# Kernel optimization log

Measured on AMD Instinct MI355X. Metric: run time of the kernel, lower is better.

## Reference

```python
import jax, jax.numpy as jnp
import numpy as np

LOG_2PI = np.float32(np.log(2.0 * np.pi))
NEG_BIG = np.float32(-9e15)


def setup_inputs() -> dict:
    key = jax.random.key(0)
    ks = jax.random.split(key, 8)
    N, F_in, F_out, H = 8192, 512, 128, 16
    x = jax.random.normal(ks[0], (N, F_in), dtype=jnp.float32)
    adj = jax.random.randint(ks[1], (N, N), 0, 2, dtype=jnp.int32)
    # xavier_uniform-ish init for W (gain 1.414)
    lim = np.float32(1.414 * np.sqrt(6.0 / (F_in + F_out)))
    W = jax.random.uniform(ks[2], (F_in, F_out), jnp.float32, -lim, lim)
    # VariationalAttentionNet params: lin1(2*F_out -> H), lin21/lin22(H -> 1)
    w1 = jax.random.normal(ks[3], (H, 2 * F_out), dtype=jnp.float32) * 0.05
    b1 = jnp.zeros((H,), jnp.float32)
    w21 = jax.random.normal(ks[4], (1, H), dtype=jnp.float32) * 0.05
    b21 = jnp.zeros((1,), jnp.float32)
    w22 = jax.random.normal(ks[5], (1, H), dtype=jnp.float32) * 0.05
    b22 = jnp.zeros((1,), jnp.float32)
    return {"x": x, "adj": adj, "W": W, "w1": w1, "b1": b1,
            "w21": w21, "b21": b21, "w22": w22, "b22": b22}


def reference(x, adj, W, w1, b1, w21, b21, w22, b22):
    # h = x @ W  [N, F_out]
    h = x @ W
    # VariationalAttentionNet(h, h), eval mode: z = mu
    u = jax.nn.relu(jnp.concatenate([h, h], axis=1) @ w1.T + b1)  # [N, H]
    mu = u @ w21.T + b21   # [N, 1]
    lv = u @ w22.T + b22   # [N, 1]
    sigma = jax.nn.softplus(lv)
    z = mu
    # qmp = -(log p(z) - log q(z)); with z = mu, log q(mu) = -log(sigma) - 0.5*log(2pi)
    log_p = jnp.sum(-0.5 * z * z - 0.5 * LOG_2PI)
    log_q = jnp.sum(-jnp.log(sigma) - 0.5 * LOG_2PI)
    qmp = log_q - log_p
    # per-node score z broadcast across row, masked by adjacency, row softmax
    scores = jnp.where(adj > 0, z, NEG_BIG)          # [N, N]
    attention = jax.nn.softmax(scores, axis=1)       # [N, N] (dropout off in eval)
    h_prime = attention @ h                          # [N, F_out]
    return jax.nn.elu(h_prime), qmp
```

## Files before the change

kernel.cpp:

```cpp
#include <hip/hip_runtime.h>

typedef unsigned int u32;
typedef unsigned short u16;

#define NN 8192
#define FIN 512
#define FOUT 128
#define NH 16
#define BK 64
#define BKA 256

typedef float f32x16 __attribute__((ext_vector_type(16)));
typedef __bf16 bf16x8 __attribute__((ext_vector_type(8)));

union PackAB { u32 u[4]; bf16x8 v; };

__device__ __forceinline__ u32 rne_hi(u32 u) {
  return u + (0x7FFFu + ((u >> 16) & 1u));
}
__device__ __forceinline__ u16 f32_to_bf16(float f) {
  return (u16)(rne_hi(__float_as_uint(f)) >> 16);
}

__global__ __launch_bounds__(256) void prep_kernel(
    const float* __restrict__ W, const float* __restrict__ w1,
    u16* __restrict__ WT, float* __restrict__ w1s) {
  int b = blockIdx.x, t = threadIdx.x;
  if (b < 256) {
    int o = b * 256 + t;
    int n = o >> 9, k = o & 511;
    WT[o] = f32_to_bf16(W[k * FOUT + n]);
  } else {
    for (int e = t; e < NH * FOUT; e += 256) {
      int k = e >> 7, f = e & 127;
      w1s[e] = w1[k * 256 + f] + w1[k * 256 + 128 + f];
    }
  }
}

__global__ __launch_bounds__(256) void h_fused_kernel(
    const float* __restrict__ x, const u16* __restrict__ WT,
    const float* __restrict__ b1, const float* __restrict__ w21,
    const float* __restrict__ b21, const float* __restrict__ w22,
    const float* __restrict__ b22, const float* __restrict__ w1s,
    u16* __restrict__ HTf, float* __restrict__ qpart) {
  __shared__ union {
    struct { u16 aS[32 * BK]; u16 bS[128 * BK]; } g;
    float hs[32][FOUT + 4];
  } S;
  __shared__ float w1l[NH][FOUT + 4];
  __shared__ float us[32][NH + 1];
  int t = threadIdx.x;
  int w = t >> 6, l = t & 63;
  int m = l & 31, kh = l >> 5;
  int i0 = blockIdx.x * 32;

  int arow = t >> 4, acol = (t & 15) * 4;
  int ac = (t & 15) >> 1, ah = t & 1;
  int aoff0 = arow * BK + ((ac ^ (arow & 7)) << 3) + ah * 4;
  int aoff1 = (arow + 16) * BK + ((ac ^ ((arow + 16) & 7)) << 3) + ah * 4;
  const float* ap0 = x + (size_t)(i0 + arow) * FIN + acol;
  const float* ap1 = ap0 + (size_t)16 * FIN;
  int hr = t >> 3, hc = t & 7;
  const u16* bp0 = WT + (size_t)hr * FIN + hc * 8;
  int boff[4];
#pragma unroll
  for (int p = 0; p < 4; ++p) {
    int r = hr + 32 * p;
    boff[p] = r * BK + ((hc ^ (r & 7)) << 3);
  }
  int aro = m * BK, am7 = m & 7;
  int nB = w * 32 + m;
  int bro = nB * BK, bm7 = nB & 7;

  float4 xa[8], xb[8];
#pragma unroll
  for (int o = 0; o < 8; ++o) {
    xa[o] = *(const float4*)(ap0 + o * BK);
    xb[o] = *(const float4*)(ap1 + o * BK);
  }
  uint4 hC[4], hN[4];
#pragma unroll
  for (int j = 0; j < 4; ++j) hC[j] = *(const uint4*)(bp0 + (size_t)(32 * j) * FIN);
  bp0 += BK;

  f32x16 acc;
#pragma unroll
  for (int r = 0; r < 16; ++r) acc[r] = 0.0f;

#pragma unroll
  for (int o = 0; o < 8; ++o) {
    if (o) __syncthreads();
    uint2 w0, w1v;
    w0.x = (rne_hi(__float_as_uint(xa[o].y)) & 0xFFFF0000u) | (rne_hi(__float_as_uint(xa[o].x)) >> 16);
    w0.y = (rne_hi(__float_as_uint(xa[o].w)) & 0xFFFF0000u) | (rne_hi(__float_as_uint(xa[o].z)) >> 16);
    w1v.x = (rne_hi(__float_as_uint(xb[o].y)) & 0xFFFF0000u) | (rne_hi(__float_as_uint(xb[o].x)) >> 16);
    w1v.y = (rne_hi(__float_as_uint(xb[o].w)) & 0xFFFF0000u) | (rne_hi(__float_as_uint(xb[o].z)) >> 16);
    *(uint2*)&S.g.aS[aoff0] = w0;
    *(uint2*)&S.g.aS[aoff1] = w1v;
#pragma unroll
    for (int j = 0; j < 4; ++j) *(uint4*)&S.g.bS[boff[j]] = hC[j];
    __syncthreads();
    if (o + 1 < 8) {
#pragma unroll
      for (int j = 0; j < 4; ++j) hN[j] = *(const uint4*)(bp0 + (size_t)(32 * j) * FIN);
      bp0 += BK;
    }
#pragma unroll
    for (int s = 0; s < BK; s += 16) {
      int cA = (s >> 3) + kh;
      PackAB pa, pb;
      pa.v = *(const bf16x8*)&S.g.aS[aro + ((cA ^ am7) << 3)];
      pb.v = *(const bf16x8*)&S.g.bS[bro + ((cA ^ bm7) << 3)];
      acc = __builtin_amdgcn_mfma_f32_32x32x16_bf16(pa.v, pb.v, acc, 0, 0, 0);
    }
    if (o + 1 < 8) {
#pragma unroll
      for (int j = 0; j < 4; ++j) hC[j] = hN[j];
    }
  }
  __syncthreads();
  {
    int col = w * 32 + m;
#pragma unroll
    for (int r = 0; r < 16; ++r) {
      int row = (r & 3) + 8 * (r >> 2) + 4 * kh;
      S.hs[row][col] = acc[r];
    }
  }
  for (int e = t; e < NH * FOUT; e += 256) w1l[e >> 7][e & 127] = w1s[e];
  __syncthreads();
  {
    int n = t & 127, g2 = t >> 7;
#pragma unroll
    for (int gg = 0; gg < 2; ++gg) {
      int g = g2 + 2 * gg;
      int k16 = (i0 >> 4) + (g >> 1), khh = g & 1;
      u32 p[4];
#pragma unroll
      for (int j = 0; j < 4; ++j) {
        u16 lo = f32_to_bf16(S.hs[g * 8 + 2 * j][n]);
        u16 hi = f32_to_bf16(S.hs[g * 8 + 2 * j + 1][n]);
        p[j] = (u32)lo | ((u32)hi << 16);
      }
      uint4 st; st.x = p[0]; st.y = p[1]; st.z = p[2]; st.w = p[3];
      size_t off = ((size_t)(k16 * 4 + (n >> 5)) * 64 + khh * 32 + (n & 31)) * 8;
      *(uint4*)(HTf + off) = st;
    }
  }
  {
    int i = t >> 3, p = t & 7;
    float s0 = b1[p], s1 = b1[p + 8];
#pragma unroll 4
    for (int f = 0; f < FOUT; ++f) {
      float hv = S.hs[i][f];
      s0 = fmaf(hv, w1l[p][f], s0);
      s1 = fmaf(hv, w1l[p + 8][f], s1);
    }
    us[i][p] = fmaxf(s0, 0.0f);
    us[i][p + 8] = fmaxf(s1, 0.0f);
  }
  __syncthreads();
  if (t < 32) {
    float mu = b21[0], lv = b22[0];
#pragma unroll
    for (int k = 0; k < NH; ++k) {
      mu = fmaf(us[t][k], w21[k], mu);
      lv = fmaf(us[t][k], w22[k], lv);
    }
    float sp = fmaxf(lv, 0.0f) + log1pf(expf(-fabsf(lv)));
    float q = 0.5f * mu * mu - logf(sp);
#pragma unroll
    for (int off = 16; off; off >>= 1) q += __shfl_down(q, off);
    if (t == 0) qpart[blockIdx.x] = q;
  }
}

__global__ __launch_bounds__(256) void attn_kernel(
    const int* __restrict__ adj, const u16* __restrict__ HTf,
    const float* __restrict__ qpart, float* __restrict__ out) {
  __shared__ u16 aS[32 * BKA];
  __shared__ float dinv[32];
  int t = threadIdx.x;
  int w = t >> 6, l = t & 63;
  int m = l & 31, kh = l >> 5;
  int i0 = blockIdx.x * 32;

  int ar = t >> 3, lc = t & 7;
  const int* apb = adj + (size_t)(i0 + ar) * NN + lc * 4;
  int woff[8];
#pragma unroll
  for (int q = 0; q < 8; ++q) {
    int c = q * 4 + (lc >> 1);
    woff[q] = ar * 256 + (((c ^ ar) & 31) << 3) + (lc & 1) * 4;
  }
  const u16* bp = HTf + (size_t)(w * 64 + l) * 8;

  f32x16 acc;
#pragma unroll
  for (int r = 0; r < 16; ++r) acc[r] = 0.0f;
  u32 degacc = 0;

  const int nslab = NN / BKA;
  int4 aC[8], aN[8];
#pragma unroll
  for (int q = 0; q < 8; ++q) aC[q] = *(const int4*)(apb + q * 32);
  apb += BKA;

  for (int o = 0; o < nslab; ++o) {
    if (o) __syncthreads();
#pragma unroll
    for (int q = 0; q < 8; ++q) {
      u32 p0 = ((u32)aC[q].y << 16) | (u32)aC[q].x;
      u32 p1 = ((u32)aC[q].w << 16) | (u32)aC[q].z;
      degacc += p0 + p1;
      uint2 wv; wv.x = p0 * 0x3F80u; wv.y = p1 * 0x3F80u;
      *(uint2*)&aS[woff[q]] = wv;
    }
    __syncthreads();
    if (o + 1 < nslab) {
#pragma unroll
      for (int q = 0; q < 8; ++q) aN[q] = *(const int4*)(apb + q * 32);
      apb += BKA;
    }
    {
      bf16x8 bF[4];
#pragma unroll
      for (int j = 0; j < 4; ++j) bF[j] = *(const bf16x8*)(bp + j * 2048);
#pragma unroll
      for (int k16 = 0; k16 < 16; k16 += 4) {
        bf16x8 bN[4];
        if (k16 + 4 < 16) {
#pragma unroll
          for (int j = 0; j < 4; ++j)
            bN[j] = *(const bf16x8*)(bp + (k16 + 4 + j) * 2048);
        }
#pragma unroll
        for (int j = 0; j < 4; ++j) {
          int cc = (k16 + j) * 2 + kh;
          PackAB pa;
          pa.v = *(const bf16x8*)&aS[m * 256 + (((cc ^ m) & 31) << 3)];
          acc = __builtin_amdgcn_mfma_f32_32x32x16_bf16(pa.v, bF[j], acc, 0, 0, 0);
        }
#pragma unroll
        for (int j = 0; j < 4; ++j) bF[j] = bN[j];
      }
    }
    bp += (size_t)16 * 2048;
#pragma unroll
    for (int q = 0; q < 8; ++q) aC[q] = aN[q];
  }
  u32 d = (degacc & 0xFFFFu) + (degacc >> 16);
  d += __shfl_down(d, 4);
  d += __shfl_down(d, 2);
  d += __shfl_down(d, 1);
  if (lc == 0) dinv[ar] = d ? 1.0f / (float)d : 0.0f;
  __syncthreads();
  int col = w * 32 + m;
#pragma unroll
  for (int r = 0; r < 16; ++r) {
    int row = (r & 3) + 8 * (r >> 2) + 4 * kh;
    float v = acc[r] * dinv[row];
    v = v > 0.0f ? v : expm1f(v);
    out[(size_t)(i0 + row) * FOUT + col] = v;
  }
  if (blockIdx.x == 0 && t < 64) {
    float v = qpart[t] + qpart[t + 64] + qpart[t + 128] + qpart[t + 192];
#pragma unroll
    for (int off = 32; off; off >>= 1) v += __shfl_down(v, off);
    if (t == 0) out[(size_t)NN * FOUT] = v;
  }
}

extern "C" void kernel_launch(void* const* d_in, const int* in_sizes, int n_in,
                              void* d_out, int out_size, void* d_ws, size_t ws_size,
                              hipStream_t stream) {
  (void)in_sizes; (void)n_in; (void)out_size; (void)ws_size;
  const float* x   = (const float*)d_in[0];
  const int*   adj = (const int*)d_in[1];
  const float* W   = (const float*)d_in[2];
  const float* w1  = (const float*)d_in[3];
  const float* b1  = (const float*)d_in[4];
  const float* w21 = (const float*)d_in[5];
  const float* b21 = (const float*)d_in[6];
  const float* w22 = (const float*)d_in[7];
  const float* b22 = (const float*)d_in[8];
  float* out = (float*)d_out;

  char* ws = (char*)d_ws;
  u16*   HTf  = (u16*)ws;   ws += (size_t)NN * FOUT * 2;
  u16*   WT   = (u16*)ws;   ws += (size_t)FOUT * FIN * 2;
  float* w1s  = (float*)ws; ws += NH * FOUT * 4;
  float* qpart= (float*)ws;

  prep_kernel<<<257, 256, 0, stream>>>(W, w1, WT, w1s);
  h_fused_kernel<<<256, 256, 0, stream>>>(x, WT, b1, w21, b21, w22, b22, w1s, HTf, qpart);
  attn_kernel<<<256, 256, 0, stream>>>(adj, HTf, qpart, out);
}
```

Measured before the change: 505.9 us.

## Split attention K dimension across four wave groups per block with LDS reduction

Each attention block now runs 1024 threads as four 256-thread groups. Each group handles a quarter of the neighbor dimension with its own LDS slab, and the partial accumulators and degree counts are combined through shared memory before normalization and ELU. The aim is more waves per CU, so more adj loads are in flight on this memory-bound 256MB adjacency stream with only 256 blocks. The cost is 64KB of LDS per block, an extra reduction pass with two barriers, and launch bounds that may limit registers.

```diff
diff --git a/kernel.cpp b/kernel.cpp
--- a/kernel.cpp
+++ b/kernel.cpp
@@ -176,32 +176,35 @@
   }
 }
 
-__global__ __launch_bounds__(256) void attn_kernel(
+__global__ __launch_bounds__(1024, 4) void attn_kernel(
     const int* __restrict__ adj, const u16* __restrict__ HTf,
     const float* __restrict__ qpart, float* __restrict__ out) {
-  __shared__ u16 aS[32 * BKA];
-  __shared__ float dinv[32];
+  __shared__ u16 aS[4 * 32 * BKA];
+  __shared__ float degp[4][32];
   int t = threadIdx.x;
-  int w = t >> 6, l = t & 63;
+  int g = t >> 8, tl = t & 255;
+  int w = tl >> 6, l = tl & 63;
   int m = l & 31, kh = l >> 5;
   int i0 = blockIdx.x * 32;
-
-  int ar = t >> 3, lc = t & 7;
-  const int* apb = adj + (size_t)(i0 + ar) * NN + lc * 4;
+  int k0 = g * (NN / 4);
+
+  int ar = tl >> 3, lc = tl & 7;
+  const int* apb = adj + (size_t)(i0 + ar) * NN + k0 + lc * 4;
+  int goff = g * 32 * BKA;
   int woff[8];
 #pragma unroll
   for (int q = 0; q < 8; ++q) {
     int c = q * 4 + (lc >> 1);
-    woff[q] = ar * 256 + (((c ^ ar) & 31) << 3) + (lc & 1) * 4;
-  }
-  const u16* bp = HTf + (size_t)(w * 64 + l) * 8;
+    woff[q] = goff + ar * 256 + (((c ^ ar) & 31) << 3) + (lc & 1) * 4;
+  }
+  const u16* bp = HTf + ((size_t)(k0 >> 4) * 4 * 64 + (size_t)(w * 64 + l)) * 8;
 
   f32x16 acc;
 #pragma unroll
   for (int r = 0; r < 16; ++r) acc[r] = 0.0f;
   u32 degacc = 0;
 
-  const int nslab = NN / BKA;
+  const int nslab = (NN / 4) / BKA;
   int4 aC[8], aN[8];
 #pragma unroll
   for (int q = 0; q < 8; ++q) aC[q] = *(const int4*)(apb + q * 32);
@@ -239,7 +242,7 @@
         for (int j = 0; j < 4; ++j) {
           int cc = (k16 + j) * 2 + kh;
           PackAB pa;
-          pa.v = *(const bf16x8*)&aS[m * 256 + (((cc ^ m) & 31) << 3)];
+          pa.v = *(const bf16x8*)&aS[goff + m * 256 + (((cc ^ m) & 31) << 3)];
           acc = __builtin_amdgcn_mfma_f32_32x32x16_bf16(pa.v, bF[j], acc, 0, 0, 0);
         }
 #pragma unroll
@@ -254,15 +257,38 @@
   d += __shfl_down(d, 4);
   d += __shfl_down(d, 2);
   d += __shfl_down(d, 1);
-  if (lc == 0) dinv[ar] = d ? 1.0f / (float)d : 0.0f;
-  __syncthreads();
-  int col = w * 32 + m;
-#pragma unroll
-  for (int r = 0; r < 16; ++r) {
-    int row = (r & 3) + 8 * (r >> 2) + 4 * kh;
-    float v = acc[r] * dinv[row];
-    v = v > 0.0f ? v : expm1f(v);
-    out[(size_t)(i0 + row) * FOUT + col] = v;
+  if (lc == 0) degp[g][ar] = (float)d;
+  __syncthreads();
+  {
+    float* accS = (float*)&aS[goff];
+    int col = w * 32 + m;
+#pragma unroll
+    for (int r = 0; r < 16; ++r) {
+      int row = (r & 3) + 8 * (r >> 2) + 4 * kh;
+      accS[row * 128 + col] = acc[r];
+    }
+  }
+  __syncthreads();
+  {
+    int idx = t * 4;
+    int row = idx >> 7;
+    const float* r0 = (const float*)aS;
+    float4 v0 = *(const float4*)(r0 + idx);
+    float4 v1 = *(const float4*)(r0 + 4096 + idx);
+    float4 v2 = *(const float4*)(r0 + 8192 + idx);
+    float4 v3 = *(const float4*)(r0 + 12288 + idx);
+    float deg = degp[0][row] + degp[1][row] + degp[2][row] + degp[3][row];
+    float rd = deg != 0.0f ? 1.0f / deg : 0.0f;
+    float4 o;
+    o.x = (v0.x + v1.x + v2.x + v3.x) * rd;
+    o.y = (v0.y + v1.y + v2.y + v3.y) * rd;
+    o.z = (v0.z + v1.z + v2.z + v3.z) * rd;
+    o.w = (v0.w + v1.w + v2.w + v3.w) * rd;
+    o.x = o.x > 0.0f ? o.x : expm1f(o.x);
+    o.y = o.y > 0.0f ? o.y : expm1f(o.y);
+    o.z = o.z > 0.0f ? o.z : expm1f(o.z);
+    o.w = o.w > 0.0f ? o.w : expm1f(o.w);
+    *(float4*)(out + (size_t)(i0 + row) * FOUT + (idx & 127)) = o;
   }
   if (blockIdx.x == 0 && t < 64) {
     float v = qpart[t] + qpart[t + 64] + qpart[t + 128] + qpart[t + 192];
@@ -295,5 +321,5 @@
 
   prep_kernel<<<257, 256, 0, stream>>>(W, w1, WT, w1s);
   h_fused_kernel<<<256, 256, 0, stream>>>(x, WT, b1, w21, b21, w22, b22, w1s, HTf, qpart);
-  attn_kernel<<<256, 256, 0, stream>>>(adj, HTf, qpart, out);
-}
+  attn_kernel<<<256, 1024, 0, stream>>>(adj, HTf, qpart, out);
+}
```

Result: faster. 449.9 us (-11.1%).

## Split attention K dimension across waves with direct register A fragments

Applied to the files above, without the earlier changes.

The attention kernel now uses 512 threads, and each of its 8 waves handles a separate K-range of the adjacency row block while computing all 128 output columns. Each wave builds its MFMA A operands straight from global adjacency loads into registers, which removes the LDS staging and the per-slab barriers. Partial accumulators and degrees are combined with shared-memory atomics before a vectorized ELU epilogue. The cost is more accumulator registers, uncoalesced per-row adjacency loads, and atomic reduction traffic in LDS.

```diff
diff --git a/kernel.cpp b/kernel.cpp
--- a/kernel.cpp
+++ b/kernel.cpp
@@ -8,7 +8,6 @@
 #define FOUT 128
 #define NH 16
 #define BK 64
-#define BKA 256
 
 typedef float f32x16 __attribute__((ext_vector_type(16)));
 typedef __bf16 bf16x8 __attribute__((ext_vector_type(8)));
@@ -176,93 +175,112 @@
   }
 }
 
-__global__ __launch_bounds__(256) void attn_kernel(
+__global__ __launch_bounds__(512, 2) void attn_kernel(
     const int* __restrict__ adj, const u16* __restrict__ HTf,
     const float* __restrict__ qpart, float* __restrict__ out) {
-  __shared__ u16 aS[32 * BKA];
-  __shared__ float dinv[32];
+  __shared__ float accS[32 * FOUT];
+  __shared__ u32 degS[32];
   int t = threadIdx.x;
   int w = t >> 6, l = t & 63;
   int m = l & 31, kh = l >> 5;
   int i0 = blockIdx.x * 32;
 
-  int ar = t >> 3, lc = t & 7;
-  const int* apb = adj + (size_t)(i0 + ar) * NN + lc * 4;
-  int woff[8];
-#pragma unroll
-  for (int q = 0; q < 8; ++q) {
-    int c = q * 4 + (lc >> 1);
-    woff[q] = ar * 256 + (((c ^ ar) & 31) << 3) + (lc & 1) * 4;
-  }
-  const u16* bp = HTf + (size_t)(w * 64 + l) * 8;
-
-  f32x16 acc;
-#pragma unroll
-  for (int r = 0; r < 16; ++r) acc[r] = 0.0f;
+  for (int e = t; e < 32 * FOUT; e += 512) accS[e] = 0.0f;
+  if (t < 32) degS[t] = 0u;
+  __syncthreads();
+
+  int k0 = w * (NN / 8);
+  const int* ap = adj + (size_t)(i0 + m) * NN + k0 + kh * 8;
+  const u16* bp = HTf + (size_t)(k0 >> 4) * 2048 + (size_t)l * 8;
+
+  f32x16 acc[4];
+#pragma unroll
+  for (int nb = 0; nb < 4; ++nb)
+#pragma unroll
+    for (int r = 0; r < 16; ++r) acc[nb][r] = 0.0f;
   u32 degacc = 0;
 
-  const int nslab = NN / BKA;
-  int4 aC[8], aN[8];
-#pragma unroll
-  for (int q = 0; q < 8; ++q) aC[q] = *(const int4*)(apb + q * 32);
-  apb += BKA;
-
-  for (int o = 0; o < nslab; ++o) {
-    if (o) __syncthreads();
-#pragma unroll
-    for (int q = 0; q < 8; ++q) {
-      u32 p0 = ((u32)aC[q].y << 16) | (u32)aC[q].x;
-      u32 p1 = ((u32)aC[q].w << 16) | (u32)aC[q].z;
-      degacc += p0 + p1;
-      uint2 wv; wv.x = p0 * 0x3F80u; wv.y = p1 * 0x3F80u;
-      *(uint2*)&aS[woff[q]] = wv;
-    }
-    __syncthreads();
-    if (o + 1 < nslab) {
-#pragma unroll
-      for (int q = 0; q < 8; ++q) aN[q] = *(const int4*)(apb + q * 32);
-      apb += BKA;
+  int4 c0 = *(const int4*)(ap);
+  int4 c1 = *(const int4*)(ap + 4);
+  int4 c2 = *(const int4*)(ap + 16);
+  int4 c3 = *(const int4*)(ap + 20);
+  ap += 32;
+
+  for (int it = 0; it < 32; ++it) {
+    int4 n0, n1, n2, n3;
+    if (it + 1 < 32) {
+      n0 = *(const int4*)(ap);
+      n1 = *(const int4*)(ap + 4);
+      n2 = *(const int4*)(ap + 16);
+      n3 = *(const int4*)(ap + 20);
+      ap += 32;
     }
     {
-      bf16x8 bF[4];
-#pragma unroll
-      for (int j = 0; j < 4; ++j) bF[j] = *(const bf16x8*)(bp + j * 2048);
-#pragma unroll
-      for (int k16 = 0; k16 < 16; k16 += 4) {
-        bf16x8 bN[4];
-        if (k16 + 4 < 16) {
-#pragma unroll
-          for (int j = 0; j < 4; ++j)
-            bN[j] = *(const bf16x8*)(bp + (k16 + 4 + j) * 2048);
-        }
-#pragma unroll
-        for (int j = 0; j < 4; ++j) {
-          int cc = (k16 + j) * 2 + kh;
-          PackAB pa;
-          pa.v = *(const bf16x8*)&aS[m * 256 + (((cc ^ m) & 31) << 3)];
-          acc = __builtin_amdgcn_mfma_f32_32x32x16_bf16(pa.v, bF[j], acc, 0, 0, 0);
-        }
-#pragma unroll
-        for (int j = 0; j < 4; ++j) bF[j] = bN[j];
+      PackAB fa;
+      u32 p0 = ((u32)c0.y << 16) | (u32)c0.x;
+      u32 p1 = ((u32)c0.w << 16) | (u32)c0.z;
+      u32 p2 = ((u32)c1.y << 16) | (u32)c1.x;
+      u32 p3 = ((u32)c1.w << 16) | (u32)c1.z;
+      degacc += p0 + p1 + p2 + p3;
+      fa.u[0] = p0 * 0x3F80u; fa.u[1] = p1 * 0x3F80u;
+      fa.u[2] = p2 * 0x3F80u; fa.u[3] = p3 * 0x3F80u;
+#pragma unroll
+      for (int nb = 0; nb < 4; ++nb) {
+        bf16x8 bf = *(const bf16x8*)(bp + nb * 512);
+        acc[nb] = __builtin_amdgcn_mfma_f32_32x32x16_bf16(fa.v, bf, acc[nb], 0, 0, 0);
       }
     }
-    bp += (size_t)16 * 2048;
-#pragma unroll
-    for (int q = 0; q < 8; ++q) aC[q] = aN[q];
-  }
-  u32 d = (degacc & 0xFFFFu) + (degacc >> 16);
-  d += __shfl_down(d, 4);
-  d += __shfl_down(d, 2);
-  d += __shfl_down(d, 1);
-  if (lc == 0) dinv[ar] = d ? 1.0f / (float)d : 0.0f;
-  __syncthreads();
-  int col = w * 32 + m;
-#pragma unroll
-  for (int r = 0; r < 16; ++r) {
-    int row = (r & 3) + 8 * (r >> 2) + 4 * kh;
-    float v = acc[r] * dinv[row];
-    v = v > 0.0f ? v : expm1f(v);
-    out[(size_t)(i0 + row) * FOUT + col] = v;
+    {
+      PackAB fb;
+      u32 p0 = ((u32)c2.y << 16) | (u32)c2.x;
+      u32 p1 = ((u32)c2.w << 16) | (u32)c2.z;
+      u32 p2 = ((u32)c3.y << 16) | (u32)c3.x;
+      u32 p3 = ((u32)c3.w << 16) | (u32)c3.z;
+      degacc += p0 + p1 + p2 + p3;
+      fb.u[0] = p0 * 0x3F80u; fb.u[1] = p1 * 0x3F80u;
+      fb.u[2] = p2 * 0x3F80u; fb.u[3] = p3 * 0x3F80u;
+#pragma unroll
+      for (int nb = 0; nb < 4; ++nb) {
+        bf16x8 bf = *(const bf16x8*)(bp + 2048 + nb * 512);
+        acc[nb] = __builtin_amdgcn_mfma_f32_32x32x16_bf16(fb.v, bf, acc[nb], 0, 0, 0);
+      }
+    }
+    bp += 4096;
+    c0 = n0; c1 = n1; c2 = n2; c3 = n3;
+  }
+  {
+    u32 d = (degacc & 0xFFFFu) + (degacc >> 16);
+    atomicAdd(&degS[m], d);
+  }
+#pragma unroll
+  for (int nb = 0; nb < 4; ++nb)
+#pragma unroll
+    for (int r = 0; r < 16; ++r) {
+      int row = (r & 3) + 8 * (r >> 2) + 4 * kh;
+      atomicAdd(&accS[row * 128 + nb * 32 + m], acc[nb][r]);
+    }
+  __syncthreads();
+  {
+    int idx = t * 8;
+    int row = idx >> 7;
+    float deg = (float)degS[row];
+    float rd = deg != 0.0f ? 1.0f / deg : 0.0f;
+    float4 v0 = *(const float4*)&accS[idx];
+    float4 v1 = *(const float4*)&accS[idx + 4];
+    float4 o0, o1;
+    o0.x = v0.x * rd; o0.y = v0.y * rd; o0.z = v0.z * rd; o0.w = v0.w * rd;
+    o1.x = v1.x * rd; o1.y = v1.y * rd; o1.z = v1.z * rd; o1.w = v1.w * rd;
+    o0.x = o0.x > 0.0f ? o0.x : expm1f(o0.x);
+    o0.y = o0.y > 0.0f ? o0.y : expm1f(o0.y);
+    o0.z = o0.z > 0.0f ? o0.z : expm1f(o0.z);
+    o0.w = o0.w > 0.0f ? o0.w : expm1f(o0.w);
+    o1.x = o1.x > 0.0f ? o1.x : expm1f(o1.x);
+    o1.y = o1.y > 0.0f ? o1.y : expm1f(o1.y);
+    o1.z = o1.z > 0.0f ? o1.z : expm1f(o1.z);
+    o1.w = o1.w > 0.0f ? o1.w : expm1f(o1.w);
+    float* op = out + (size_t)(i0 + row) * FOUT + (idx & 127);
+    *(float4*)op = o0;
+    *(float4*)(op + 4) = o1;
   }
   if (blockIdx.x == 0 && t < 64) {
     float v = qpart[t] + qpart[t + 64] + qpart[t + 128] + qpart[t + 192];
@@ -295,5 +313,5 @@
 
   prep_kernel<<<257, 256, 0, stream>>>(W, w1, WT, w1s);
   h_fused_kernel<<<256, 256, 0, stream>>>(x, WT, b1, w21, b21, w22, b22, w1s, HTf, qpart);
-  attn_kernel<<<256, 256, 0, stream>>>(adj, HTf, qpart, out);
-}
+  attn_kernel<<<256, 512, 0, stream>>>(adj, HTf, qpart, out);
+}
```

After: 504.5 us. Within noise of the previous version (-0.3%).

## Split attention reduction dimension across blocks and add a separate reduce kernel

Applied to the files above, without the earlier changes.

The attention matmul is split along the K (neighbour) dimension into up to four chunks, so the grid grows from 256 blocks to 256*KSA and fills more compute units. Each block writes partial row sums and partial degree counts to workspace. A new reduce kernel adds the partials, normalises by degree, applies ELU and computes the qmp scalar. The cost is extra global traffic for the partial buffers, one more kernel launch, and reliance on the workspace being large enough (KSA drops back if it is not).

```diff
diff --git a/kernel.cpp b/kernel.cpp
--- a/kernel.cpp
+++ b/kernel.cpp
@@ -176,32 +176,32 @@
   }
 }
 
-__global__ __launch_bounds__(256) void attn_kernel(
+__global__ __launch_bounds__(256, 4) void attn_kernel(
     const int* __restrict__ adj, const u16* __restrict__ HTf,
-    const float* __restrict__ qpart, float* __restrict__ out) {
+    float* __restrict__ Sp, u32* __restrict__ degw, int KL) {
   __shared__ u16 aS[32 * BKA];
-  __shared__ float dinv[32];
   int t = threadIdx.x;
   int w = t >> 6, l = t & 63;
   int m = l & 31, kh = l >> 5;
-  int i0 = blockIdx.x * 32;
+  int tile = blockIdx.x & 255, chunk = blockIdx.x >> 8;
+  int i0 = tile * 32, k0 = chunk * KL;
 
   int ar = t >> 3, lc = t & 7;
-  const int* apb = adj + (size_t)(i0 + ar) * NN + lc * 4;
+  const int* apb = adj + (size_t)(i0 + ar) * NN + k0 + lc * 4;
   int woff[8];
 #pragma unroll
   for (int q = 0; q < 8; ++q) {
     int c = q * 4 + (lc >> 1);
     woff[q] = ar * 256 + (((c ^ ar) & 31) << 3) + (lc & 1) * 4;
   }
-  const u16* bp = HTf + (size_t)(w * 64 + l) * 8;
+  const u16* bp = HTf + ((size_t)(k0 >> 4) * 4 * 64 + (size_t)(w * 64 + l)) * 8;
 
   f32x16 acc;
 #pragma unroll
   for (int r = 0; r < 16; ++r) acc[r] = 0.0f;
   u32 degacc = 0;
 
-  const int nslab = NN / BKA;
+  int nslab = KL / BKA;
   int4 aC[8], aN[8];
 #pragma unroll
   for (int q = 0; q < 8; ++q) aC[q] = *(const int4*)(apb + q * 32);
@@ -254,28 +254,53 @@
   d += __shfl_down(d, 4);
   d += __shfl_down(d, 2);
   d += __shfl_down(d, 1);
-  if (lc == 0) dinv[ar] = d ? 1.0f / (float)d : 0.0f;
-  __syncthreads();
+  if (lc == 0) degw[chunk * NN + i0 + ar] = d;
+  float* sp = Sp + (size_t)chunk * NN * FOUT;
   int col = w * 32 + m;
 #pragma unroll
   for (int r = 0; r < 16; ++r) {
     int row = (r & 3) + 8 * (r >> 2) + 4 * kh;
-    float v = acc[r] * dinv[row];
-    v = v > 0.0f ? v : expm1f(v);
-    out[(size_t)(i0 + row) * FOUT + col] = v;
-  }
-  if (blockIdx.x == 0 && t < 64) {
-    float v = qpart[t] + qpart[t + 64] + qpart[t + 128] + qpart[t + 192];
+    sp[(size_t)(i0 + row) * FOUT + col] = acc[r];
+  }
+}
+
+__global__ __launch_bounds__(256) void reduceSq_kernel(
+    const float* __restrict__ Sp, const u32* __restrict__ degw,
+    const float* __restrict__ qpart, float* __restrict__ out, int KSA) {
+  int t = threadIdx.x;
+  if (blockIdx.x == 1024) {
+    __shared__ float sred[4];
+    float v = qpart[t];
 #pragma unroll
     for (int off = 32; off; off >>= 1) v += __shfl_down(v, off);
-    if (t == 0) out[(size_t)NN * FOUT] = v;
-  }
+    if ((t & 63) == 0) sred[t >> 6] = v;
+    __syncthreads();
+    if (t == 0) out[(size_t)NN * FOUT] = sred[0] + sred[1] + sred[2] + sred[3];
+    return;
+  }
+  int idx = (blockIdx.x * 256 + t) * 4;
+  int i = idx >> 7;
+  u32 deg = 0;
+  for (int c = 0; c < KSA; ++c) deg += degw[c * NN + i];
+  float4 s = {0.0f, 0.0f, 0.0f, 0.0f};
+  for (int c = 0; c < KSA; ++c) {
+    float4 v4 = *(const float4*)(Sp + (size_t)c * NN * FOUT + idx);
+    s.x += v4.x; s.y += v4.y; s.z += v4.z; s.w += v4.w;
+  }
+  float rd = deg ? 1.0f / (float)deg : 0.0f;
+  float4 o;
+  o.x = s.x * rd; o.y = s.y * rd; o.z = s.z * rd; o.w = s.w * rd;
+  o.x = o.x > 0.0f ? o.x : expm1f(o.x);
+  o.y = o.y > 0.0f ? o.y : expm1f(o.y);
+  o.z = o.z > 0.0f ? o.z : expm1f(o.z);
+  o.w = o.w > 0.0f ? o.w : expm1f(o.w);
+  *(float4*)(out + idx) = o;
 }
 
 extern "C" void kernel_launch(void* const* d_in, const int* in_sizes, int n_in,
                               void* d_out, int out_size, void* d_ws, size_t ws_size,
                               hipStream_t stream) {
-  (void)in_sizes; (void)n_in; (void)out_size; (void)ws_size;
+  (void)in_sizes; (void)n_in; (void)out_size;
   const float* x   = (const float*)d_in[0];
   const int*   adj = (const int*)d_in[1];
   const float* W   = (const float*)d_in[2];
@@ -287,13 +312,28 @@
   const float* b22 = (const float*)d_in[8];
   float* out = (float*)d_out;
 
+  const size_t TILE4 = (size_t)NN * FOUT * 4;
+  int KSA = 4;
+  for (;;) {
+    size_t need = (size_t)KSA * TILE4
+                + (size_t)NN * FOUT * 2
+                + (size_t)FOUT * FIN * 2
+                + (size_t)KSA * NN * 4
+                + NH * FOUT * 4 + 2048;
+    if (need <= ws_size || KSA == 1) break;
+    KSA >>= 1;
+  }
+
   char* ws = (char*)d_ws;
-  u16*   HTf  = (u16*)ws;   ws += (size_t)NN * FOUT * 2;
-  u16*   WT   = (u16*)ws;   ws += (size_t)FOUT * FIN * 2;
-  float* w1s  = (float*)ws; ws += NH * FOUT * 4;
+  float* Sp   = (float*)ws;                          ws += (size_t)KSA * TILE4;
+  u16*   HTf  = (u16*)ws;                            ws += (size_t)NN * FOUT * 2;
+  u16*   WT   = (u16*)ws;                            ws += (size_t)FOUT * FIN * 2;
+  u32*   degw = (u32*)ws;                            ws += (size_t)KSA * NN * 4;
+  float* w1s  = (float*)ws;                          ws += NH * FOUT * 4;
   float* qpart= (float*)ws;
 
   prep_kernel<<<257, 256, 0, stream>>>(W, w1, WT, w1s);
   h_fused_kernel<<<256, 256, 0, stream>>>(x, WT, b1, w21, b21, w22, b22, w1s, HTf, qpart);
-  attn_kernel<<<256, 256, 0, stream>>>(adj, HTf, qpart, out);
-}
+  attn_kernel<<<256 * KSA, 256, 0, stream>>>(adj, HTf, Sp, degw, NN / KSA);
+  reduceSq_kernel<<<1025, 256, 0, stream>>>(Sp, degw, qpart, out, KSA);
+}
```

Result: faster. 432.7 us (-14.5%).
